# Kernel optimization log

Hardware: AMD Instinct MI355X
Metric: run time of the kernel (lower is better)

The kernel has to match this reference:

```python
import jax, jax.numpy as jnp
import numpy as np

H = 32        # num_heads
E = 128       # hidden_dim (per-head K/V/query dim)
D_STATE = 512 # encoder state width
B, LQ, LK = 8, 1024, 1024


def setup_inputs() -> dict:
    key = jax.random.key(0)
    ks = jax.random.split(key, 8)
    query = jax.random.normal(ks[0], (B, LQ, E), dtype=jnp.float32)
    states = jax.random.normal(ks[1], (B, LK, D_STATE), dtype=jnp.float32)
    s = 1.0 / np.sqrt(D_STATE)
    Wk = jax.random.uniform(ks[2], (H, D_STATE, E), minval=-s, maxval=s, dtype=jnp.float32)
    bk = jax.random.uniform(ks[3], (H, E), minval=-s, maxval=s, dtype=jnp.float32)
    Wv = jax.random.uniform(ks[4], (H, D_STATE, E), minval=-s, maxval=s, dtype=jnp.float32)
    bv = jax.random.uniform(ks[5], (H, E), minval=-s, maxval=s, dtype=jnp.float32)
    so = 1.0 / np.sqrt(H * E)
    Wo = jax.random.uniform(ks[6], (H * E, E), minval=-so, maxval=so, dtype=jnp.float32)
    bo = jax.random.uniform(ks[7], (E,), minval=-so, maxval=so, dtype=jnp.float32)
    return {"query": query, "states": states, "Wk": Wk, "bk": bk,
            "Wv": Wv, "bv": bv, "Wo": Wo, "bo": bo}


def reference(query, states, Wk, bk, Wv, bv, Wo, bo):
    # Per-head K/V projections of the shared states: [H,B,Lk,E]
    keys = jnp.einsum('bkd,hde->hbke', states, Wk) + bk[:, None, None, :]
    values = jnp.einsum('bkd,hde->hbke', states, Wv) + bv[:, None, None, :]
    # Scaled dot-product scores: [H,B,Lq,Lk]
    scale = 1.0 / jnp.sqrt(jnp.asarray(E, dtype=query.dtype))
    scores = jnp.einsum('bqe,hbke->hbqk', query, keys) * scale
    # Original detaches the softmax output before AV
    attn = jax.lax.stop_gradient(jax.nn.softmax(scores, axis=-1))
    ctx = jnp.einsum('hbqk,hbke->hbqe', attn, values)       # [H,B,Lq,E]
    # concat heads along last dim: [B,Lq,H*E]
    ctx = jnp.transpose(ctx, (1, 2, 0, 3)).reshape(query.shape[0], query.shape[1], -1)
    return ctx @ Wo + bo
```

## Files before the change

kernel.cpp:

```cpp
#include <hip/hip_runtime.h>

#define H_  32
#define E_  128
#define D_  512
#define B_  8
#define LQ_ 1024
#define LK_ 1024

typedef __bf16 bf16x8 __attribute__((ext_vector_type(8)));
typedef float  f32x4  __attribute__((ext_vector_type(4)));
typedef float  f32x16 __attribute__((ext_vector_type(16)));

typedef __attribute__((address_space(1))) const unsigned int guint;
typedef __attribute__((address_space(3))) unsigned int luint;

__device__ __forceinline__ f32x4 MFMA16(bf16x8 a, bf16x8 b, f32x4 c) {
    return __builtin_amdgcn_mfma_f32_16x16x32_bf16(a, b, c, 0, 0, 0);
}
__device__ __forceinline__ f32x16 MFMA32(bf16x8 a, bf16x8 b, f32x16 c) {
    return __builtin_amdgcn_mfma_f32_32x32x16_bf16(a, b, c, 0, 0, 0);
}

__device__ __forceinline__ unsigned short f2bf(float x) {
    union { float f; unsigned u; } v; v.f = x;
    unsigned r = v.u + 0x7fffu + ((v.u >> 16) & 1u);
    return (unsigned short)(r >> 16);
}
__device__ __forceinline__ unsigned pkbf(float a, float b) {
    union { float f; unsigned u; } x, y; x.f = a; y.f = b;
    return __builtin_amdgcn_perm(y.u, x.u, 0x07060302u);
}

__global__ void conv_scale_kernel(const float* __restrict__ in,
                                  unsigned short* __restrict__ out,
                                  long n4, float scale) {
    long i = blockIdx.x * (long)blockDim.x + threadIdx.x;
    long stride = (long)gridDim.x * blockDim.x;
    for (; i < n4; i += stride) {
        float4 v = ((const float4*)in)[i];
        union { unsigned long long u; unsigned short s[4]; } p;
        p.s[0] = f2bf(v.x * scale); p.s[1] = f2bf(v.y * scale);
        p.s[2] = f2bf(v.z * scale); p.s[3] = f2bf(v.w * scale);
        ((unsigned long long*)out)[i] = p.u;
    }
}

__global__ void transpose_bf16_kernel(const float* __restrict__ in,
                                      unsigned short* __restrict__ out,
                                      int R, int C, long inStride, long outStride) {
    in  += (long)blockIdx.z * inStride;
    out += (long)blockIdx.z * outStride;
    __shared__ float t[32][33];
    int x = threadIdx.x, y = threadIdx.y;
    int c0 = blockIdx.x * 32, r0 = blockIdx.y * 32;
    for (int i = 0; i < 32; i += 8) t[y + i][x] = in[(long)(r0 + y + i) * C + (c0 + x)];
    __syncthreads();
    for (int i = 0; i < 32; i += 8)
        out[(long)(c0 + y + i) * R + (r0 + x)] = f2bf(t[x][y + i]);
}

__global__ __launch_bounds__(512, 4) void kv_proj_kernel(
    const unsigned short* __restrict__ sb,
    const unsigned short* __restrict__ wkt,
    const unsigned short* __restrict__ wvt,
    const float* __restrict__ bk, const float* __restrict__ bv,
    unsigned short* __restrict__ Kb,
    unsigned short* __restrict__ Vtb)
{
    int bid = blockIdx.x;
    const int x = bid & 7;  int s = bid >> 3;
    const int mt = s & 3;   s >>= 2;
    const int b  = s & 7;   s >>= 3;
    const int kv = s & 1;   s >>= 1;
    const int h  = s * 8 + x;

    const unsigned short* wt = kv ? wvt : wkt;
    const float* bias = kv ? bv : bk;

    __shared__ unsigned short As[2][256 * 32];
    __shared__ unsigned short Bs[2][128 * 32];

    const int tid = threadIdx.x;
    const int wave = tid >> 6, lane = tid & 63;
    const int ln = lane & 31, hi = lane >> 5;
    const int wm = wave & 3, wn = wave >> 2;

    const unsigned short* Ag = sb + ((long)b * LK_ + mt * 256) * D_;
    const unsigned short* Bg = wt + (long)h * E_ * D_;

    int aoff[2], boff;
    #pragma unroll
    for (int d = 0; d < 2; d++) {
        int row = (wave * 2 + d) * 16 + (lane >> 2);
        int ch  = (lane & 3) ^ ((row >> 1) & 3);
        aoff[d] = row * D_ + ch * 8;
    }
    {
        int row = wave * 16 + (lane >> 2);
        int ch  = (lane & 3) ^ ((row >> 1) & 3);
        boff = row * D_ + ch * 8;
    }

    #define KV_STAGE(d0_, buf_)                                                     \
        do {                                                                        \
            _Pragma("unroll")                                                       \
            for (int d = 0; d < 2; d++)                                             \
                __builtin_amdgcn_global_load_lds(                                   \
                    (guint*)(Ag + aoff[d] + (d0_)),                                 \
                    (luint*)&As[buf_][(wave * 2 + d) * 512], 16, 0, 0);             \
            __builtin_amdgcn_global_load_lds(                                       \
                (guint*)(Bg + boff + (d0_)),                                        \
                (luint*)&Bs[buf_][wave * 512], 16, 0, 0);                           \
        } while (0)

    KV_STAGE(0, 0);
    __syncthreads();

    f32x16 acc[4] = {};

    for (int it = 0; it < 16; it++) {
        const int buf = it & 1;
        if (it < 15) KV_STAGE((it + 1) * 32, buf ^ 1);

        #pragma unroll
        for (int ss = 0; ss < 2; ss++) {
            const int c = ss * 2 + hi;
            bf16x8 af[2], bfr[2];
            #pragma unroll
            for (int mb = 0; mb < 2; mb++) {
                const int r = wm * 64 + mb * 32 + ln;
                af[mb] = *(const bf16x8*)&As[buf][r * 32 + (c ^ ((r >> 1) & 3)) * 8];
            }
            #pragma unroll
            for (int nb = 0; nb < 2; nb++) {
                const int r = wn * 64 + nb * 32 + ln;
                bfr[nb] = *(const bf16x8*)&Bs[buf][r * 32 + (c ^ ((r >> 1) & 3)) * 8];
            }
            #pragma unroll
            for (int mb = 0; mb < 2; mb++)
                #pragma unroll
                for (int nb = 0; nb < 2; nb++)
                    acc[mb * 2 + nb] = MFMA32(af[mb], bfr[nb], acc[mb * 2 + nb]);
        }
        __syncthreads();
    }

    const int row0 = mt * 256 + wm * 64;
    const int e0 = wn * 64;
    if (!kv) {
        const long base = ((long)h * B_ + b) * LK_;
        #pragma unroll
        for (int mb = 0; mb < 2; mb++)
            #pragma unroll
            for (int nb = 0; nb < 2; nb++) {
                const int e = e0 + nb * 32 + ln;
                const float be = bias[h * E_ + e];
                #pragma unroll
                for (int r = 0; r < 16; r++) {
                    int row = row0 + mb * 32 + (r & 3) + 8 * (r >> 2) + 4 * hi;
                    Kb[(base + row) * E_ + e] = f2bf(acc[mb * 2 + nb][r] + be);
                }
            }
    } else {
        const long vbase = ((long)h * B_ + b) * E_;
        #pragma unroll
        for (int mb = 0; mb < 2; mb++)
            #pragma unroll
            for (int nb = 0; nb < 2; nb++) {
                const int e = e0 + nb * 32 + ln;
                const float be = bias[h * E_ + e];
                #pragma unroll
                for (int rg = 0; rg < 4; rg++) {
                    int k0 = row0 + mb * 32 + 8 * rg + 4 * hi;
                    union { unsigned long long u; unsigned short s2[4]; } pk;
                    #pragma unroll
                    for (int j = 0; j < 4; j++)
                        pk.s2[j] = f2bf(acc[mb * 2 + nb][rg * 4 + j] + be);
                    *(unsigned long long*)&Vtb[(vbase + e) * (long)LK_ + k0] = pk.u;
                }
            }
    }
}

__global__ __launch_bounds__(256, 3) void attn_kernel(
    const unsigned short* __restrict__ qb,
    const unsigned short* __restrict__ Kb,
    const unsigned short* __restrict__ Vtb,
    unsigned short* __restrict__ ctx)
{
    int bid = blockIdx.x;
    const int b = bid & 7;
    int s = bid >> 3;
    const int qt = s & 7;
    const int h  = s >> 3;

    __shared__ unsigned short Ks[64 * 128];
    __shared__ unsigned short Vs[2][128 * 64];

    const int tid = threadIdx.x;
    const int wave = tid >> 6, lane = tid & 63;
    const int ln = lane & 31, hi = lane >> 5;

    const unsigned short* Kg = Kb  + ((long)h * B_ + b) * (long)LK_ * E_;
    const unsigned short* Vg = Vtb + ((long)h * B_ + b) * (long)E_ * LK_;
    const int qrow = qt * 128 + wave * 32;

    bf16x8 qf[8];
    #pragma unroll
    for (int s8 = 0; s8 < 8; s8++) {
        union { uint4 u; bf16x8 v; } t;
        t.u = *(const uint4*)&qb[((long)b * LQ_ + qrow + ln) * E_ + s8 * 16 + hi * 8];
        qf[s8] = t.v;
    }

    int koff[4], voff[4];
    #pragma unroll
    for (int d = 0; d < 4; d++) {
        int krow = (wave * 4 + d) * 4 + (lane >> 4);
        int kc = (lane & 15) ^ (krow & 15);
        koff[d] = krow * E_ + kc * 8;
        int vrow = (wave * 4 + d) * 8 + (lane >> 3);
        int vc = (lane & 7) ^ (vrow & 7);
        voff[d] = vrow * LK_ + vc * 8;
    }

    #define STAGE_K(t_)                                                             \
        do {                                                                        \
            _Pragma("unroll")                                                       \
            for (int d = 0; d < 4; d++)                                             \
                __builtin_amdgcn_global_load_lds(                                   \
                    (guint*)(Kg + (long)(t_) * (64 * E_) + koff[d]),                \
                    (luint*)&Ks[(wave * 4 + d) * 512], 16, 0, 0);                   \
        } while (0)
    #define STAGE_V(t_, buf_)                                                       \
        do {                                                                        \
            _Pragma("unroll")                                                       \
            for (int d = 0; d < 4; d++)                                             \
                __builtin_amdgcn_global_load_lds(                                   \
                    (guint*)(Vg + (t_) * 64 + voff[d]),                             \
                    (luint*)&Vs[buf_][(wave * 4 + d) * 512], 16, 0, 0);             \
        } while (0)

    STAGE_K(0);
    STAGE_V(0, 0);
    __syncthreads();

    f32x16 O[4] = {};
    float l_run = 0.f;

    for (int t = 0; t < 16; t++) {
        const int vb = t & 1;

        f32x16 S[2] = {};
        #pragma unroll
        for (int es = 0; es < 8; es++) {
            #pragma unroll
            for (int mb = 0; mb < 2; mb++) {
                const int row = mb * 32 + ln;
                const int cs = (es * 2 + hi) ^ (row & 15);
                bf16x8 kf = *(const bf16x8*)&Ks[row * 128 + cs * 8];
                S[mb] = MFMA32(kf, qf[es], S[mb]);
            }
        }

        __syncthreads();
        if (t < 15) {
            STAGE_K(t + 1);
            STAGE_V(t + 1, vb ^ 1);
        }

        float tsum = 0.f;
        #pragma unroll
        for (int mb = 0; mb < 2; mb++) {
            float pv[16];
            #pragma unroll
            for (int r = 0; r < 16; r++) {
                pv[r] = __builtin_amdgcn_exp2f(S[mb][r]);
                tsum += pv[r];
            }
            unsigned a0 = pkbf(pv[0],  pv[1]),  b0 = pkbf(pv[2],  pv[3]);
            unsigned a1 = pkbf(pv[4],  pv[5]),  b1 = pkbf(pv[6],  pv[7]);
            unsigned a2 = pkbf(pv[8],  pv[9]),  b2 = pkbf(pv[10], pv[11]);
            unsigned a3 = pkbf(pv[12], pv[13]), b3 = pkbf(pv[14], pv[15]);
            unsigned r0 = __shfl_xor(hi ? a0 : a1, 32, 64);
            unsigned r1 = __shfl_xor(hi ? b0 : b1, 32, 64);
            unsigned r2 = __shfl_xor(hi ? a2 : a3, 32, 64);
            unsigned r3 = __shfl_xor(hi ? b2 : b3, 32, 64);
            #pragma unroll
            for (int st = 0; st < 2; st++) {
                union { unsigned u[4]; bf16x8 v; } pa;
                if (st == 0) {
                    pa.u[0] = hi ? r0 : a0;  pa.u[1] = hi ? r1 : b0;
                    pa.u[2] = hi ? a1 : r0;  pa.u[3] = hi ? b1 : r1;
                } else {
                    pa.u[0] = hi ? r2 : a2;  pa.u[1] = hi ? r3 : b2;
                    pa.u[2] = hi ? a3 : r2;  pa.u[3] = hi ? b3 : r3;
                }
                #pragma unroll
                for (int nb = 0; nb < 4; nb++) {
                    const int vrow = nb * 32 + ln;
                    const int vc = (mb * 4 + st * 2 + hi) ^ (vrow & 7);
                    bf16x8 vf = *(const bf16x8*)&Vs[vb][vrow * 64 + vc * 8];
                    O[nb] = MFMA32(pa.v, vf, O[nb]);
                }
            }
        }
        tsum += __shfl_xor(tsum, 32, 64);
        l_run += tsum;

        __syncthreads();
    }

    const float linv = 1.f / l_run;
    #pragma unroll
    for (int r = 0; r < 16; r++) {
        const int rowmap = (r & 3) + 8 * (r >> 2) + 4 * hi;
        float lv = __shfl(linv, rowmap, 64);
        int qg = qrow + rowmap;
        long rowbase = ((long)b * LQ_ + qg) * (H_ * E_) + h * E_;
        #pragma unroll
        for (int nb = 0; nb < 4; nb++)
            ctx[rowbase + nb * 32 + ln] = f2bf(O[nb][r] * lv);
    }
}

__global__ void init_out_kernel(float* __restrict__ out, const float* __restrict__ bo) {
    int i = blockIdx.x * blockDim.x + threadIdx.x;
    float4 b4 = ((const float4*)bo)[i & 31];
    ((float4*)out)[i] = b4;
}

__global__ __launch_bounds__(256) void out_proj_kernel(
    const unsigned short* __restrict__ ctx,
    const unsigned short* __restrict__ wot,
    float* __restrict__ out)
{
    const int qt = blockIdx.x;
    const int kc = blockIdx.y;
    __shared__ unsigned short As[128 * 72];
    __shared__ unsigned short Bs[128 * 72];
    const int tid = threadIdx.x;
    const int wave = tid >> 6, lane = tid & 63;
    const int lq = lane & 15, quad = lane >> 4;
    const long kbase = (long)kc * 512;

    f32x4 acc[2][8] = {};

    for (int d0 = 0; d0 < 512; d0 += 64) {
        __syncthreads();
        for (int i = 0; i < 4; i++) {
            int g = i * 256 + tid;
            int row = g >> 3, cc = (g & 7) * 8;
            *(uint4*)&As[row * 72 + cc] =
                *(const uint4*)&ctx[(long)(qt * 128 + row) * (H_ * E_) + kbase + d0 + cc];
            *(uint4*)&Bs[row * 72 + cc] =
                *(const uint4*)&wot[(long)row * (H_ * E_) + kbase + d0 + cc];
        }
        __syncthreads();
        for (int ds = 0; ds < 64; ds += 32) {
            bf16x8 a0 = *(const bf16x8*)&As[(wave * 32 + lq) * 72 + ds + quad * 8];
            bf16x8 a1 = *(const bf16x8*)&As[(wave * 32 + 16 + lq) * 72 + ds + quad * 8];
            for (int et = 0; et < 8; et++) {
                bf16x8 bb = *(const bf16x8*)&Bs[(et * 16 + lq) * 72 + ds + quad * 8];
                acc[0][et] = MFMA16(a0, bb, acc[0][et]);
                acc[1][et] = MFMA16(a1, bb, acc[1][et]);
            }
        }
    }
    for (int kt = 0; kt < 2; kt++)
        for (int et = 0; et < 8; et++)
            for (int r = 0; r < 4; r++) {
                int q = qt * 128 + wave * 32 + kt * 16 + quad * 4 + r;
                int eo = et * 16 + lq;
                atomicAdd(&out[(long)q * E_ + eo], acc[kt][et][r]);
            }
}

extern "C" void kernel_launch(void* const* d_in, const int* in_sizes, int n_in,
                              void* d_out, int out_size, void* d_ws, size_t ws_size,
                              hipStream_t stream) {
    const float* query  = (const float*)d_in[0];
    const float* states = (const float*)d_in[1];
    const float* Wk     = (const float*)d_in[2];
    const float* bk     = (const float*)d_in[3];
    const float* Wv     = (const float*)d_in[4];
    const float* bv     = (const float*)d_in[5];
    const float* Wo     = (const float*)d_in[6];
    const float* bo     = (const float*)d_in[7];
    float* out = (float*)d_out;

    const size_t WS_QB  = 0;
    const size_t WS_SB  = WS_QB  + 2097152UL;
    const size_t WS_WKT = WS_SB  + 8388608UL;
    const size_t WS_WVT = WS_WKT + 4194304UL;
    const size_t WS_WOT = WS_WVT + 4194304UL;
    const size_t WS_KB  = WS_WOT + 1048576UL;
    const size_t WS_VTB = WS_KB  + 67108864UL;
    const size_t WS_CTX = WS_VTB + 67108864UL;
    const size_t WS_END = WS_CTX + 67108864UL;
    if (ws_size < WS_END) return;

    char* ws = (char*)d_ws;
    unsigned short* qb  = (unsigned short*)(ws + WS_QB);
    unsigned short* sb  = (unsigned short*)(ws + WS_SB);
    unsigned short* wkt = (unsigned short*)(ws + WS_WKT);
    unsigned short* wvt = (unsigned short*)(ws + WS_WVT);
    unsigned short* wot = (unsigned short*)(ws + WS_WOT);
    unsigned short* Kb  = (unsigned short*)(ws + WS_KB);
    unsigned short* Vtb = (unsigned short*)(ws + WS_VTB);
    unsigned short* ctx = (unsigned short*)(ws + WS_CTX);

    const float SCALE = 0.12751744f;

    conv_scale_kernel<<<512, 256, 0, stream>>>(query, qb, (long)(B_ * LQ_ * E_ / 4), SCALE);
    conv_scale_kernel<<<1024, 256, 0, stream>>>(states, sb, (long)(B_ * LK_ * D_ / 4), 1.0f);
    transpose_bf16_kernel<<<dim3(4, 16, 32), dim3(32, 8), 0, stream>>>(
        Wk, wkt, D_, E_, (long)D_ * E_, (long)D_ * E_);
    transpose_bf16_kernel<<<dim3(4, 16, 32), dim3(32, 8), 0, stream>>>(
        Wv, wvt, D_, E_, (long)D_ * E_, (long)D_ * E_);
    transpose_bf16_kernel<<<dim3(4, 128, 1), dim3(32, 8), 0, stream>>>(
        Wo, wot, H_ * E_, E_, 0L, 0L);

    kv_proj_kernel<<<2048, 512, 0, stream>>>(sb, wkt, wvt, bk, bv, Kb, Vtb);
    attn_kernel<<<2048, 256, 0, stream>>>(qb, Kb, Vtb, ctx);

    init_out_kernel<<<1024, 256, 0, stream>>>(out, bo);
    out_proj_kernel<<<dim3(64, 8), 256, 0, stream>>>(ctx, wot, out);
}
```

Before: 398.3 us.

## Replace split-K atomic out-projection with double-buffered direct-to-LDS GEMM and fused bias

```diff
diff --git a/kernel.cpp b/kernel.cpp
--- a/kernel.cpp
+++ b/kernel.cpp
@@ -324,56 +324,85 @@
     }
 }
 
-__global__ void init_out_kernel(float* __restrict__ out, const float* __restrict__ bo) {
-    int i = blockIdx.x * blockDim.x + threadIdx.x;
-    float4 b4 = ((const float4*)bo)[i & 31];
-    ((float4*)out)[i] = b4;
-}
-
-__global__ __launch_bounds__(256) void out_proj_kernel(
+__global__ __launch_bounds__(512) void out_proj_kernel(
     const unsigned short* __restrict__ ctx,
     const unsigned short* __restrict__ wot,
+    const float* __restrict__ bo,
     float* __restrict__ out)
 {
     const int qt = blockIdx.x;
-    const int kc = blockIdx.y;
-    __shared__ unsigned short As[128 * 72];
-    __shared__ unsigned short Bs[128 * 72];
+    __shared__ unsigned short As[2][32 * 128];
+    __shared__ unsigned short Bs[2][128 * 128];
+
     const int tid = threadIdx.x;
     const int wave = tid >> 6, lane = tid & 63;
-    const int lq = lane & 15, quad = lane >> 4;
-    const long kbase = (long)kc * 512;
-
-    f32x4 acc[2][8] = {};
-
-    for (int d0 = 0; d0 < 512; d0 += 64) {
+    const int l16 = lane & 15, l4 = lane >> 4;
+    const int wm = wave >> 2, wn = wave & 3;
+
+    const unsigned short* Ag = ctx + (long)(qt * 32) * (H_ * E_);
+
+    long goff[5]; int isB[5], dbase[5];
+    #pragma unroll
+    for (int i = 0; i < 5; i++) {
+        int d  = wave * 5 + i;
+        int bB = (d >= 8);
+        int dd = bB ? d - 8 : d;
+        int r  = dd * 4 + l4;
+        int sc = l16 ^ (r & 7);
+        goff[i]  = (long)r * (H_ * E_) + sc * 8;
+        isB[i]   = bB;
+        dbase[i] = dd * 512;
+    }
+
+    #define OP_STAGE(k0_, buf_)                                                     \
+        do {                                                                        \
+            _Pragma("unroll")                                                       \
+            for (int i = 0; i < 5; i++) {                                           \
+                if (isB[i])                                                         \
+                    __builtin_amdgcn_global_load_lds(                               \
+                        (guint*)(wot + goff[i] + (k0_)),                            \
+                        (luint*)&Bs[buf_][dbase[i]], 16, 0, 0);                     \
+                else                                                                \
+                    __builtin_amdgcn_global_load_lds(                               \
+                        (guint*)(Ag + goff[i] + (k0_)),                             \
+                        (luint*)&As[buf_][dbase[i]], 16, 0, 0);                     \
+            }                                                                       \
+        } while (0)
+
+    OP_STAGE(0, 0);
+    __syncthreads();
+
+    f32x4 acc[2] = {};
+
+    for (int kt = 0; kt < 32; kt++) {
+        const int buf = kt & 1;
+        if (kt < 31) OP_STAGE((kt + 1) * 128, buf ^ 1);
+
+        const int ar = wm * 16 + l16;
+        #pragma unroll
+        for (int ks = 0; ks < 4; ks++) {
+            const int sl = ks * 4 + l4;
+            bf16x8 af = *(const bf16x8*)&As[buf][ar * 128 + (sl ^ (ar & 7)) * 8];
+            #pragma unroll
+            for (int nb = 0; nb < 2; nb++) {
+                const int br = wn * 32 + nb * 16 + l16;
+                bf16x8 bf = *(const bf16x8*)&Bs[buf][br * 128 + (sl ^ (br & 7)) * 8];
+                acc[nb] = MFMA16(af, bf, acc[nb]);
+            }
+        }
         __syncthreads();
-        for (int i = 0; i < 4; i++) {
-            int g = i * 256 + tid;
-            int row = g >> 3, cc = (g & 7) * 8;
-            *(uint4*)&As[row * 72 + cc] =
-                *(const uint4*)&ctx[(long)(qt * 128 + row) * (H_ * E_) + kbase + d0 + cc];
-            *(uint4*)&Bs[row * 72 + cc] =
-                *(const uint4*)&wot[(long)row * (H_ * E_) + kbase + d0 + cc];
-        }
-        __syncthreads();
-        for (int ds = 0; ds < 64; ds += 32) {
-            bf16x8 a0 = *(const bf16x8*)&As[(wave * 32 + lq) * 72 + ds + quad * 8];
-            bf16x8 a1 = *(const bf16x8*)&As[(wave * 32 + 16 + lq) * 72 + ds + quad * 8];
-            for (int et = 0; et < 8; et++) {
-                bf16x8 bb = *(const bf16x8*)&Bs[(et * 16 + lq) * 72 + ds + quad * 8];
-                acc[0][et] = MFMA16(a0, bb, acc[0][et]);
-                acc[1][et] = MFMA16(a1, bb, acc[1][et]);
-            }
-        }
-    }
-    for (int kt = 0; kt < 2; kt++)
-        for (int et = 0; et < 8; et++)
-            for (int r = 0; r < 4; r++) {
-                int q = qt * 128 + wave * 32 + kt * 16 + quad * 4 + r;
-                int eo = et * 16 + lq;
-                atomicAdd(&out[(long)q * E_ + eo], acc[kt][et][r]);
-            }
+    }
+
+    #pragma unroll
+    for (int nb = 0; nb < 2; nb++) {
+        const int e = wn * 32 + nb * 16 + l16;
+        const float be = bo[e];
+        #pragma unroll
+        for (int r = 0; r < 4; r++) {
+            int m = qt * 32 + wm * 16 + l4 * 4 + r;
+            out[(long)m * E_ + e] = acc[nb][r] + be;
+        }
+    }
 }
 
 extern "C" void kernel_launch(void* const* d_in, const int* in_sizes, int n_in,
@@ -424,6 +453,5 @@
     kv_proj_kernel<<<2048, 512, 0, stream>>>(sb, wkt, wvt, bk, bv, Kb, Vtb);
     attn_kernel<<<2048, 256, 0, stream>>>(qb, Kb, Vtb, ctx);
 
-    init_out_kernel<<<1024, 256, 0, stream>>>(out, bo);
-    out_proj_kernel<<<dim3(64, 8), 256, 0, stream>>>(ctx, wot, out);
-}
+    out_proj_kernel<<<256, 512, 0, stream>>>(ctx, wot, bo, out);
+}
```

New measurement: 386.1 us. 1.03x faster.
